# Kernel tuning notes

Hardware: AMD Instinct MI355X
Metric: run time of the kernel (lower is better)

Reference implementation:

```python
import jax, jax.numpy as jnp
import numpy as np

OUT = 4096       # out_features
IN = 4096        # in_features
GS = 128         # group_size
G = IN // GS     # num_groups = 32 (IN divisible by GS -> no padding path)


def setup_inputs() -> dict:
    key = jax.random.key(0)
    k1, k2, k3 = jax.random.split(key, 3)
    x = jax.random.normal(k1, (4096, IN), dtype=jnp.float32)
    # packed int4 weights: each byte holds two 4-bit codes in [0,15] (offset-8)
    qweight = jax.random.randint(k2, (OUT, IN // 2), 0, 256, dtype=jnp.int32)
    # per-(row, group) positive scales
    scale = jax.random.uniform(k3, (OUT, G, 1), dtype=jnp.float32,
                               minval=0.01, maxval=0.1)
    return {"x": x, "qweight": qweight, "scale": scale}


def reference(x, qweight, scale):
    # unpack_int4: high nibble is the even-position element, low nibble odd
    high = (qweight >> 4) & 15
    low = qweight & 15
    q = jnp.stack([high, low], axis=-1).reshape(OUT, -1)  # [OUT, IN]
    q = q.astype(jnp.float32) - 8.0                       # back to [-8, 7]
    # group-wise dequantization
    w = q.reshape(OUT, G, GS) * scale                     # [OUT, G, GS]
    B = x.shape[0]
    xg = x.reshape(B, G, GS)                              # [B, G, GS]
    return jnp.einsum('bgs,ogs->bo', xg, w)               # [B, OUT]
```

## Files before the change

kernel.cpp:

```cpp
#include <hip/hip_runtime.h>

typedef __attribute__((ext_vector_type(8))) _Float16 f16x8;
typedef __attribute__((ext_vector_type(4))) float    f32x4;
typedef __attribute__((ext_vector_type(4))) int      i32x4;

#define IN_F   4096
#define OUT_F  4096
#define NGRP   32
#define NKT    64

#define GLOAD16(gsrc, ldst)                                                   \
    __builtin_amdgcn_global_load_lds(                                         \
        (const __attribute__((address_space(1))) unsigned int*)(gsrc),        \
        (__attribute__((address_space(3))) unsigned int*)(ldst), 16, 0, 0)

#define CFENCE  asm volatile("" ::: "memory")
#define BARRIER do { CFENCE; __builtin_amdgcn_s_barrier(); CFENCE; } while (0)
#define VMW6    asm volatile("s_waitcnt vmcnt(6)" ::: "memory")

__global__ __launch_bounds__(256)
void prep(const float* __restrict__ X, const int* __restrict__ QW,
          const float* __restrict__ S, _Float16* __restrict__ XF,
          _Float16* __restrict__ WF) {
    if (blockIdx.x < 8192) {
        size_t i = ((size_t)blockIdx.x * 256 + threadIdx.x) * 8;
        f32x4 a = *(const f32x4*)(X + i);
        f32x4 b = *(const f32x4*)(X + i + 4);
        f16x8 h;
        h[0] = (_Float16)a[0]; h[1] = (_Float16)a[1];
        h[2] = (_Float16)a[2]; h[3] = (_Float16)a[3];
        h[4] = (_Float16)b[0]; h[5] = (_Float16)b[1];
        h[6] = (_Float16)b[2]; h[7] = (_Float16)b[3];
        *(f16x8*)(XF + i) = h;
    } else {
        size_t t  = ((size_t)blockIdx.x - 8192) * 256 + threadIdx.x;
        size_t jj = t * 4;
        size_t o  = jj >> 11;
        size_t jr = jj & 2047;
        const float s = S[o * NGRP + (jr >> 6)];
        i32x4 q = *(const i32x4*)(QW + jj);
        f16x8 h;
#pragma unroll
        for (int j = 0; j < 4; ++j) {
            const int v = q[j];
            h[2 * j]     = (_Float16)((float)(((v >> 4) & 15) - 8) * s);
            h[2 * j + 1] = (_Float16)((float)((v & 15) - 8) * s);
        }
        *(f16x8*)(WF + jj * 2) = h;
    }
}

__global__ __launch_bounds__(512, 2)
void gemm8p(const _Float16* __restrict__ A,
            const _Float16* __restrict__ B,
            float*          __restrict__ C)
{
    extern __shared__ char LDSc[];
    char* const ldsA = LDSc;
    char* const ldsB = LDSc + 65536;

    const int tid  = threadIdx.x;
    const int lane = tid & 63;
    const int wid  = tid >> 6;
    const int wm   = wid >> 2;
    const int wn   = wid & 3;

    const int bid = blockIdx.x;
    const int swz = (bid & 7) * 32 + (bid >> 3);
    const int bm0 = (swz >> 4) * 256;
    const int bn0 = (swz & 15) * 256;

    const int r0 = tid >> 3;
    const int cs = ((tid & 7) * 16) ^ ((r0 & 7) << 4);
    const _Float16* Asrc = A + (size_t)(bm0 + r0) * IN_F + (cs >> 1);
    const _Float16* Bsrc = B + (size_t)(bn0 + r0) * IN_F + (cs >> 1);
    const int dstoff = wid * 1024;

    const int lane15 = lane & 15;
    const int swr = (lane & 7) << 4;
    const int c0 = ((lane >> 4) * 16) ^ swr;
    const int c1 = (64 + (lane >> 4) * 16) ^ swr;
    int rAoff[4], rBoff[2];
#pragma unroll
    for (int mm = 0; mm < 4; ++mm) rAoff[mm] = (wm * 64 + mm * 16 + lane15) * 128;
#pragma unroll
    for (int nn = 0; nn < 2; ++nn) rBoff[nn] = (wn * 32 + nn * 16 + lane15) * 128;

    f16x8 afr[4][2], blo[2][2], bhi[2][2];
    f32x4 acc[8][4];
#pragma unroll
    for (int m = 0; m < 8; ++m)
#pragma unroll
        for (int n = 0; n < 4; ++n) acc[m][n] = (f32x4)0.0f;

#define STAGE_A(HALF, KT, BUF) do {                                           \
        const _Float16* s_ = Asrc + (size_t)(HALF) * 128 * IN_F + (KT) * 64;  \
        char* d_ = ldsA + ((BUF) * 2 + (HALF)) * 16384 + dstoff;              \
        GLOAD16(s_, d_);                                                      \
        GLOAD16(s_ + (size_t)64 * IN_F, d_ + 8192); } while (0)

#define STAGE_B(HALF, KT, BUF) do {                                           \
        const _Float16* s_ = Bsrc + (size_t)(HALF) * 128 * IN_F + (KT) * 64;  \
        char* d_ = ldsB + ((BUF) * 2 + (HALF)) * 16384 + dstoff;              \
        GLOAD16(s_, d_);                                                      \
        GLOAD16(s_ + (size_t)64 * IN_F, d_ + 8192); } while (0)

#define RD_A(BUF, QM) do { char* ab_ = ldsA + ((BUF) * 2 + (QM)) * 16384;     \
        _Pragma("unroll") for (int mm = 0; mm < 4; ++mm) {                    \
            afr[mm][0] = *(const f16x8*)(ab_ + rAoff[mm] + c0);               \
            afr[mm][1] = *(const f16x8*)(ab_ + rAoff[mm] + c1); } } while (0)

#define RD_B(BUF, QN, DST) do { char* bb_ = ldsB + ((BUF) * 2 + (QN)) * 16384;\
        _Pragma("unroll") for (int nn = 0; nn < 2; ++nn) {                    \
            DST[nn][0] = *(const f16x8*)(bb_ + rBoff[nn] + c0);               \
            DST[nn][1] = *(const f16x8*)(bb_ + rBoff[nn] + c1); } } while (0)

#define MFMA_Q(QM, QN, BQ)                                                    \
        __builtin_amdgcn_s_setprio(1);                                        \
        _Pragma("unroll") for (int mm = 0; mm < 4; ++mm)                      \
        _Pragma("unroll") for (int nn = 0; nn < 2; ++nn)                      \
        _Pragma("unroll") for (int kk = 0; kk < 2; ++kk)                      \
            acc[(QM)*4+mm][(QN)*2+nn] =                                       \
                __builtin_amdgcn_mfma_f32_16x16x32_f16(                       \
                    afr[mm][kk], BQ[nn][kk], acc[(QM)*4+mm][(QN)*2+nn],0,0,0);\
        __builtin_amdgcn_s_setprio(0);

    STAGE_A(0, 0, 0); STAGE_B(0, 0, 0); STAGE_B(1, 0, 0); STAGE_A(1, 0, 0);
    STAGE_A(0, 1, 1); STAGE_B(0, 1, 1); STAGE_B(1, 1, 1);
    VMW6; BARRIER;

    for (int t = 0; t < NKT; t += 2) {
        const int k2 = (t + 2) & 63;
        const int k3 = (t + 3) & 63;
        RD_A(0, 0); RD_B(0, 0, blo); RD_B(0, 1, bhi);
        STAGE_A(1, t + 1, 1);
        MFMA_Q(0, 0, blo); MFMA_Q(0, 1, bhi);
        BARRIER;
        RD_A(0, 1);
        STAGE_A(0, k2, 0); STAGE_B(0, k2, 0); STAGE_B(1, k2, 0);
        MFMA_Q(1, 0, blo); MFMA_Q(1, 1, bhi);
        VMW6; BARRIER;
        RD_A(1, 0); RD_B(1, 0, blo); RD_B(1, 1, bhi);
        STAGE_A(1, k2, 0);
        MFMA_Q(0, 0, blo); MFMA_Q(0, 1, bhi);
        BARRIER;
        RD_A(1, 1);
        STAGE_A(0, k3, 1); STAGE_B(0, k3, 1); STAGE_B(1, k3, 1);
        MFMA_Q(1, 0, blo); MFMA_Q(1, 1, bhi);
        VMW6; BARRIER;
    }
    asm volatile("s_waitcnt vmcnt(0)" ::: "memory");

#pragma unroll
    for (int m = 0; m < 8; ++m) {
        const int Mr = bm0 + (m >> 2) * 128 + wm * 64 + (m & 3) * 16 + (lane >> 4) * 4;
#pragma unroll
        for (int n = 0; n < 4; ++n) {
            const int Nc = bn0 + (n >> 1) * 128 + wn * 32 + (n & 1) * 16 + lane15;
#pragma unroll
            for (int r = 0; r < 4; ++r)
                C[(size_t)(Mr + r) * OUT_F + Nc] = acc[m][n][r];
        }
    }
#undef STAGE_A
#undef STAGE_B
#undef RD_A
#undef RD_B
#undef MFMA_Q
}

__global__ __launch_bounds__(256, 3)
void gemm_f16(const _Float16* __restrict__ A,
              const _Float16* __restrict__ B,
              float*          __restrict__ C)
{
    __shared__ __align__(16) _Float16 lA[128 * 32];
    __shared__ __align__(16) _Float16 lB[128 * 32];

    const int tid  = threadIdx.x;
    const int lane = tid & 63;
    const int bid = blockIdx.x;
    const int swz = (bid & 7) * 128 + (bid >> 3);
    const int bm0 = (swz >> 5) * 128;
    const int bn0 = (swz & 31) * 128;

    const int sr = tid >> 2;
    const int sc = (tid & 3) * 8;
    const _Float16* Aps = A + (size_t)(bm0 + sr) * IN_F + sc;
    const _Float16* Bps = B + (size_t)(bn0 + sr) * IN_F + sc;
    char* lAb = (char*)lA + (tid & ~63) * 16;
    char* lBb = (char*)lB + (tid & ~63) * 16;

    const int wv = tid >> 6;
    const int wr = (wv >> 1) * 64;
    const int wc = (wv & 1)  * 64;
    const int lr  = lane & 15;
    const int lkb = (lane >> 4) * 16;

    f32x4 acc[4][4];
#pragma unroll
    for (int m = 0; m < 4; ++m)
#pragma unroll
        for (int n = 0; n < 4; ++n) acc[m][n] = (f32x4)0.0f;

    for (int kt = 0; kt < 128; ++kt) {
        __syncthreads();
        {
            const _Float16* ak = Aps + kt * 32;
            const _Float16* bk = Bps + kt * 32;
            GLOAD16(ak, lAb);
            GLOAD16(ak + (size_t)64 * IN_F, lAb + 4096);
            GLOAD16(bk, lBb);
            GLOAD16(bk + (size_t)64 * IN_F, lBb + 4096);
        }
        __syncthreads();

        f16x8 a[4], b[4];
#pragma unroll
        for (int m = 0; m < 4; ++m)
            a[m] = *(const f16x8*)((const char*)lA + (wr + m * 16 + lr) * 64 + lkb);
#pragma unroll
        for (int n = 0; n < 4; ++n)
            b[n] = *(const f16x8*)((const char*)lB + (wc + n * 16 + lr) * 64 + lkb);
#pragma unroll
        for (int m = 0; m < 4; ++m)
#pragma unroll
            for (int n = 0; n < 4; ++n)
                acc[m][n] = __builtin_amdgcn_mfma_f32_16x16x32_f16(
                    a[m], b[n], acc[m][n], 0, 0, 0);
    }

    const int crow = bm0 + wr + (lane >> 4) * 4;
    const int ccol = bn0 + wc + lr;
#pragma unroll
    for (int m = 0; m < 4; ++m)
#pragma unroll
        for (int n = 0; n < 4; ++n)
#pragma unroll
            for (int r = 0; r < 4; ++r)
                C[(size_t)(crow + m * 16 + r) * OUT_F + (ccol + n * 16)]
                    = acc[m][n][r];
}

extern "C" void kernel_launch(void* const* d_in, const int* in_sizes, int n_in,
                              void* d_out, int out_size, void* d_ws, size_t ws_size,
                              hipStream_t stream) {
    (void)in_sizes; (void)n_in; (void)out_size; (void)ws_size;
    const float* x  = (const float*)d_in[0];
    const int*   qw = (const int*)d_in[1];
    const float* s  = (const float*)d_in[2];
    float*       out = (float*)d_out;

    _Float16* xf = (_Float16*)d_ws;
    _Float16* wf = xf + (size_t)OUT_F * IN_F;
    prep<<<dim3(16384), dim3(256), 0, stream>>>(x, qw, s, xf, wf);

    hipError_t e = hipFuncSetAttribute((const void*)gemm8p,
        hipFuncAttributeMaxDynamicSharedMemorySize, 131072);
    if (e == hipSuccess)
        gemm8p<<<dim3(256), dim3(512), 131072, stream>>>(xf, wf, out);
    else
        gemm_f16<<<dim3(1024), dim3(256), 0, stream>>>(xf, wf, out);
}
```

Baseline: 135.4 us.

## Load A fragments directly from global into registers, triple-buffer B in LDS

```diff
diff --git a/kernel.cpp b/kernel.cpp
--- a/kernel.cpp
+++ b/kernel.cpp
@@ -16,7 +16,7 @@
 
 #define CFENCE  asm volatile("" ::: "memory")
 #define BARRIER do { CFENCE; __builtin_amdgcn_s_barrier(); CFENCE; } while (0)
-#define VMW6    asm volatile("s_waitcnt vmcnt(6)" ::: "memory")
+#define VMW4    asm volatile("s_waitcnt vmcnt(4)" ::: "memory")
 
 __global__ __launch_bounds__(256)
 void prep(const float* __restrict__ X, const int* __restrict__ QW,
@@ -51,13 +51,11 @@
 }
 
 __global__ __launch_bounds__(512, 2)
-void gemm8p(const _Float16* __restrict__ A,
-            const _Float16* __restrict__ B,
-            float*          __restrict__ C)
+void gemm_ad(const _Float16* __restrict__ A,
+             const _Float16* __restrict__ B,
+             float*          __restrict__ C)
 {
-    extern __shared__ char LDSc[];
-    char* const ldsA = LDSc;
-    char* const ldsB = LDSc + 65536;
+    extern __shared__ char ldsB[];
 
     const int tid  = threadIdx.x;
     const int lane = tid & 63;
@@ -72,7 +70,6 @@
 
     const int r0 = tid >> 3;
     const int cs = ((tid & 7) * 16) ^ ((r0 & 7) << 4);
-    const _Float16* Asrc = A + (size_t)(bm0 + r0) * IN_F + (cs >> 1);
     const _Float16* Bsrc = B + (size_t)(bn0 + r0) * IN_F + (cs >> 1);
     const int dstoff = wid * 1024;
 
@@ -80,93 +77,78 @@
     const int swr = (lane & 7) << 4;
     const int c0 = ((lane >> 4) * 16) ^ swr;
     const int c1 = (64 + (lane >> 4) * 16) ^ swr;
-    int rAoff[4], rBoff[2];
-#pragma unroll
-    for (int mm = 0; mm < 4; ++mm) rAoff[mm] = (wm * 64 + mm * 16 + lane15) * 128;
-#pragma unroll
-    for (int nn = 0; nn < 2; ++nn) rBoff[nn] = (wn * 32 + nn * 16 + lane15) * 128;
-
-    f16x8 afr[4][2], blo[2][2], bhi[2][2];
+    int rBoff[4];
+#pragma unroll
+    for (int nn = 0; nn < 4; ++nn) rBoff[nn] = (wn * 64 + nn * 16 + lane15) * 128;
+
+    const _Float16* Ap[8];
+#pragma unroll
+    for (int m = 0; m < 8; ++m)
+        Ap[m] = A + (size_t)(bm0 + wm * 128 + m * 16 + lane15) * IN_F
+                  + (lane >> 4) * 8;
+
+    f16x8 a[8][2], b[4][2];
     f32x4 acc[8][4];
 #pragma unroll
     for (int m = 0; m < 8; ++m)
 #pragma unroll
         for (int n = 0; n < 4; ++n) acc[m][n] = (f32x4)0.0f;
 
-#define STAGE_A(HALF, KT, BUF) do {                                           \
-        const _Float16* s_ = Asrc + (size_t)(HALF) * 128 * IN_F + (KT) * 64;  \
-        char* d_ = ldsA + ((BUF) * 2 + (HALF)) * 16384 + dstoff;              \
-        GLOAD16(s_, d_);                                                      \
-        GLOAD16(s_ + (size_t)64 * IN_F, d_ + 8192); } while (0)
-
-#define STAGE_B(HALF, KT, BUF) do {                                           \
-        const _Float16* s_ = Bsrc + (size_t)(HALF) * 128 * IN_F + (KT) * 64;  \
-        char* d_ = ldsB + ((BUF) * 2 + (HALF)) * 16384 + dstoff;              \
-        GLOAD16(s_, d_);                                                      \
-        GLOAD16(s_ + (size_t)64 * IN_F, d_ + 8192); } while (0)
-
-#define RD_A(BUF, QM) do { char* ab_ = ldsA + ((BUF) * 2 + (QM)) * 16384;     \
-        _Pragma("unroll") for (int mm = 0; mm < 4; ++mm) {                    \
-            afr[mm][0] = *(const f16x8*)(ab_ + rAoff[mm] + c0);               \
-            afr[mm][1] = *(const f16x8*)(ab_ + rAoff[mm] + c1); } } while (0)
-
-#define RD_B(BUF, QN, DST) do { char* bb_ = ldsB + ((BUF) * 2 + (QN)) * 16384;\
-        _Pragma("unroll") for (int nn = 0; nn < 2; ++nn) {                    \
-            DST[nn][0] = *(const f16x8*)(bb_ + rBoff[nn] + c0);               \
-            DST[nn][1] = *(const f16x8*)(bb_ + rBoff[nn] + c1); } } while (0)
-
-#define MFMA_Q(QM, QN, BQ)                                                    \
-        __builtin_amdgcn_s_setprio(1);                                        \
-        _Pragma("unroll") for (int mm = 0; mm < 4; ++mm)                      \
-        _Pragma("unroll") for (int nn = 0; nn < 2; ++nn)                      \
-        _Pragma("unroll") for (int kk = 0; kk < 2; ++kk)                      \
-            acc[(QM)*4+mm][(QN)*2+nn] =                                       \
-                __builtin_amdgcn_mfma_f32_16x16x32_f16(                       \
-                    afr[mm][kk], BQ[nn][kk], acc[(QM)*4+mm][(QN)*2+nn],0,0,0);\
+#define STAGE_B(KT, BUF) do {                                                 \
+        _Pragma("unroll") for (int j = 0; j < 4; ++j)                         \
+            GLOAD16(Bsrc + (size_t)j * 64 * IN_F + (KT) * 64,                 \
+                    ldsB + (BUF) * 32768 + dstoff + j * 8192); } while (0)
+
+    STAGE_B(0, 0); STAGE_B(1, 1);
+    VMW4; BARRIER;
+
+    int cur = 0;
+    for (int t = 0; t < NKT; ++t) {
+        const int nx2 = (cur == 0) ? 2 : cur - 1;
+#pragma unroll
+        for (int m = 0; m < 8; ++m) {
+            const _Float16* ap = Ap[m] + t * 64;
+            a[m][0] = *(const f16x8*)(ap);
+            a[m][1] = *(const f16x8*)(ap + 32);
+        }
+        CFENCE;
+        STAGE_B((t + 2) & 63, nx2);
+        CFENCE;
+        {
+            char* bb = ldsB + cur * 32768;
+#pragma unroll
+            for (int nn = 0; nn < 4; ++nn) {
+                b[nn][0] = *(const f16x8*)(bb + rBoff[nn] + c0);
+                b[nn][1] = *(const f16x8*)(bb + rBoff[nn] + c1);
+            }
+        }
+        __builtin_amdgcn_s_setprio(1);
+#pragma unroll
+        for (int m = 0; m < 8; ++m)
+#pragma unroll
+            for (int nn = 0; nn < 4; ++nn)
+#pragma unroll
+                for (int kk = 0; kk < 2; ++kk)
+                    acc[m][nn] = __builtin_amdgcn_mfma_f32_16x16x32_f16(
+                        a[m][kk], b[nn][kk], acc[m][nn], 0, 0, 0);
         __builtin_amdgcn_s_setprio(0);
-
-    STAGE_A(0, 0, 0); STAGE_B(0, 0, 0); STAGE_B(1, 0, 0); STAGE_A(1, 0, 0);
-    STAGE_A(0, 1, 1); STAGE_B(0, 1, 1); STAGE_B(1, 1, 1);
-    VMW6; BARRIER;
-
-    for (int t = 0; t < NKT; t += 2) {
-        const int k2 = (t + 2) & 63;
-        const int k3 = (t + 3) & 63;
-        RD_A(0, 0); RD_B(0, 0, blo); RD_B(0, 1, bhi);
-        STAGE_A(1, t + 1, 1);
-        MFMA_Q(0, 0, blo); MFMA_Q(0, 1, bhi);
-        BARRIER;
-        RD_A(0, 1);
-        STAGE_A(0, k2, 0); STAGE_B(0, k2, 0); STAGE_B(1, k2, 0);
-        MFMA_Q(1, 0, blo); MFMA_Q(1, 1, bhi);
-        VMW6; BARRIER;
-        RD_A(1, 0); RD_B(1, 0, blo); RD_B(1, 1, bhi);
-        STAGE_A(1, k2, 0);
-        MFMA_Q(0, 0, blo); MFMA_Q(0, 1, bhi);
-        BARRIER;
-        RD_A(1, 1);
-        STAGE_A(0, k3, 1); STAGE_B(0, k3, 1); STAGE_B(1, k3, 1);
-        MFMA_Q(1, 0, blo); MFMA_Q(1, 1, bhi);
-        VMW6; BARRIER;
+        VMW4; BARRIER;
+        cur = (cur == 2) ? 0 : cur + 1;
     }
     asm volatile("s_waitcnt vmcnt(0)" ::: "memory");
 
 #pragma unroll
     for (int m = 0; m < 8; ++m) {
-        const int Mr = bm0 + (m >> 2) * 128 + wm * 64 + (m & 3) * 16 + (lane >> 4) * 4;
-#pragma unroll
-        for (int n = 0; n < 4; ++n) {
-            const int Nc = bn0 + (n >> 1) * 128 + wn * 32 + (n & 1) * 16 + lane15;
+        const int Mr = bm0 + wm * 128 + m * 16 + (lane >> 4) * 4;
+#pragma unroll
+        for (int nn = 0; nn < 4; ++nn) {
+            const int Nc = bn0 + wn * 64 + nn * 16 + lane15;
 #pragma unroll
             for (int r = 0; r < 4; ++r)
-                C[(size_t)(Mr + r) * OUT_F + Nc] = acc[m][n][r];
-        }
-    }
-#undef STAGE_A
+                C[(size_t)(Mr + r) * OUT_F + Nc] = acc[m][nn][r];
+        }
+    }
 #undef STAGE_B
-#undef RD_A
-#undef RD_B
-#undef MFMA_Q
 }
 
 __global__ __launch_bounds__(256, 3)
@@ -255,10 +237,10 @@
     _Float16* wf = xf + (size_t)OUT_F * IN_F;
     prep<<<dim3(16384), dim3(256), 0, stream>>>(x, qw, s, xf, wf);
 
-    hipError_t e = hipFuncSetAttribute((const void*)gemm8p,
-        hipFuncAttributeMaxDynamicSharedMemorySize, 131072);
+    hipError_t e = hipFuncSetAttribute((const void*)gemm_ad,
+        hipFuncAttributeMaxDynamicSharedMemorySize, 98304);
     if (e == hipSuccess)
-        gemm8p<<<dim3(256), dim3(512), 131072, stream>>>(xf, wf, out);
+        gemm_ad<<<dim3(256), dim3(512), 98304, stream>>>(xf, wf, out);
     else
         gemm_f16<<<dim3(1024), dim3(256), 0, stream>>>(xf, wf, out);
 }
```

New measurement: 327.8 us. 2.42x slower.

## Add 256x128-tile triple-buffered GEMM with two blocks per CU

Applied to the files above, without the earlier changes.

```diff
diff --git a/kernel.cpp b/kernel.cpp
--- a/kernel.cpp
+++ b/kernel.cpp
@@ -7,7 +7,6 @@
 #define IN_F   4096
 #define OUT_F  4096
 #define NGRP   32
-#define NKT    64
 
 #define GLOAD16(gsrc, ldst)                                                   \
     __builtin_amdgcn_global_load_lds(                                         \
@@ -50,6 +49,95 @@
     }
 }
 
+__global__ __launch_bounds__(256, 2)
+void gemm_tlp(const _Float16* __restrict__ A,
+              const _Float16* __restrict__ B,
+              float*          __restrict__ C)
+{
+    extern __shared__ char LDSc[];
+    char* const ldsA = LDSc;
+    char* const ldsB = LDSc + 49152;
+
+    const int tid  = threadIdx.x;
+    const int lane = tid & 63;
+    const int wid  = tid >> 6;
+    const int wm   = wid >> 1;
+    const int wn   = wid & 1;
+
+    const int bid = blockIdx.x;
+    const int swz = (bid & 7) * 64 + (bid >> 3);
+    const int bm0 = (swz >> 5) * 256;
+    const int bn0 = (swz & 31) * 128;
+
+    const _Float16* Asrc = A + (size_t)(bm0 + tid) * IN_F;
+    const _Float16* Bsrc = B + (size_t)(bn0 + (tid & 127)) * IN_F + (tid >> 7) * 8;
+    const int dstoff = wid * 1024;
+
+    const int lane15 = lane & 15;
+    const int ks     = lane >> 4;
+    int aoff[8], boff[4];
+#pragma unroll
+    for (int m = 0; m < 8; ++m)
+        aoff[m] = (ks * 256 + wm * 128 + m * 16 + lane15) * 16;
+#pragma unroll
+    for (int n = 0; n < 4; ++n)
+        boff[n] = (ks * 128 + wn * 64 + n * 16 + lane15) * 16;
+
+    f16x8 a[8], b[4];
+    f32x4 acc[8][4];
+#pragma unroll
+    for (int m = 0; m < 8; ++m)
+#pragma unroll
+        for (int n = 0; n < 4; ++n) acc[m][n] = (f32x4)0.0f;
+
+#define STAGE(KT, R) do {                                                     \
+        _Pragma("unroll") for (int c = 0; c < 4; ++c)                         \
+            GLOAD16(Asrc + (KT) * 32 + c * 8,                                 \
+                    ldsA + (R) * 16384 + c * 4096 + dstoff);                  \
+        _Pragma("unroll") for (int c = 0; c < 2; ++c)                         \
+            GLOAD16(Bsrc + (KT) * 32 + c * 16,                                \
+                    ldsB + (R) * 8192 + c * 4096 + dstoff); } while (0)
+
+    STAGE(0, 0); STAGE(1, 1);
+    VMW6; BARRIER;
+
+    int r0 = 0;
+    for (int t = 0; t < 128; ++t) {
+        int r2 = r0 + 2; if (r2 >= 3) r2 -= 3;
+        char* ab = ldsA + r0 * 16384;
+        char* bb = ldsB + r0 * 8192;
+#pragma unroll
+        for (int m = 0; m < 8; ++m) a[m] = *(const f16x8*)(ab + aoff[m]);
+#pragma unroll
+        for (int n = 0; n < 4; ++n) b[n] = *(const f16x8*)(bb + boff[n]);
+        STAGE((t + 2) & 127, r2);
+        __builtin_amdgcn_s_setprio(1);
+#pragma unroll
+        for (int m = 0; m < 8; ++m)
+#pragma unroll
+            for (int n = 0; n < 4; ++n)
+                acc[m][n] = __builtin_amdgcn_mfma_f32_16x16x32_f16(
+                    a[m], b[n], acc[m][n], 0, 0, 0);
+        __builtin_amdgcn_s_setprio(0);
+        VMW6; BARRIER;
+        r0 = (r0 == 2) ? 0 : r0 + 1;
+    }
+    asm volatile("s_waitcnt vmcnt(0)" ::: "memory");
+
+#pragma unroll
+    for (int m = 0; m < 8; ++m) {
+        const int Mr = bm0 + wm * 128 + m * 16 + ks * 4;
+#pragma unroll
+        for (int n = 0; n < 4; ++n) {
+            const int Nc = bn0 + wn * 64 + n * 16 + lane15;
+#pragma unroll
+            for (int r = 0; r < 4; ++r)
+                C[(size_t)(Mr + r) * OUT_F + Nc] = acc[m][n][r];
+        }
+    }
+#undef STAGE
+}
+
 __global__ __launch_bounds__(512, 2)
 void gemm8p(const _Float16* __restrict__ A,
             const _Float16* __restrict__ B,
@@ -129,7 +217,7 @@
     STAGE_A(0, 1, 1); STAGE_B(0, 1, 1); STAGE_B(1, 1, 1);
     VMW6; BARRIER;
 
-    for (int t = 0; t < NKT; t += 2) {
+    for (int t = 0; t < 64; t += 2) {
         const int k2 = (t + 2) & 63;
         const int k3 = (t + 3) & 63;
         RD_A(0, 0); RD_B(0, 0, blo); RD_B(0, 1, bhi);
@@ -255,9 +343,15 @@
     _Float16* wf = xf + (size_t)OUT_F * IN_F;
     prep<<<dim3(16384), dim3(256), 0, stream>>>(x, qw, s, xf, wf);
 
-    hipError_t e = hipFuncSetAttribute((const void*)gemm8p,
+    hipError_t e1 = hipFuncSetAttribute((const void*)gemm_tlp,
+        hipFuncAttributeMaxDynamicSharedMemorySize, 73728);
+    if (e1 == hipSuccess) {
+        gemm_tlp<<<dim3(512), dim3(256), 73728, stream>>>(xf, wf, out);
+        return;
+    }
+    hipError_t e2 = hipFuncSetAttribute((const void*)gemm8p,
         hipFuncAttributeMaxDynamicSharedMemorySize, 131072);
-    if (e == hipSuccess)
+    if (e2 == hipSuccess)
         gemm8p<<<dim3(256), dim3(512), 131072, stream>>>(xf, wf, out);
     else
         gemm_f16<<<dim3(1024), dim3(256), 0, stream>>>(xf, wf, out);
```

New measurement: 259.4 us. 91.6% more time.
